# Performance work log

Measured on AMD Instinct MI355X. Metric: run time of the kernel, lower is better.

## Reference

```python
import jax, jax.numpy as jnp
import numpy as np
import math

IN_FEATURES = 1024
OUT_FEATURES = 1024
RANK = 16
ALPHA = 16.0
SCALING = ALPHA / RANK


def setup_inputs() -> dict:
    key = jax.random.key(0)
    k_x, k_w, k_b, k_a, k_bb = jax.random.split(key, 5)
    x = jax.random.normal(k_x, (8, 4096, IN_FEATURES), dtype=jnp.float32)
    # frozen linear params (W: [out, in], b: [out])
    W = jax.random.normal(k_w, (OUT_FEATURES, IN_FEATURES), dtype=jnp.float32) / math.sqrt(IN_FEATURES)
    b = jax.random.normal(k_b, (OUT_FEATURES,), dtype=jnp.float32) * 0.01
    # kaiming-uniform-like init for A; B nonzero here so the LoRA path is exercised
    bound = 1.0 / math.sqrt(IN_FEATURES)
    lora_A = jax.random.uniform(k_a, (RANK, IN_FEATURES), minval=-bound, maxval=bound, dtype=jnp.float32)
    lora_B = jax.random.normal(k_bb, (OUT_FEATURES, RANK), dtype=jnp.float32) * 0.02
    return {"x": x, "W": W, "b": b, "lora_A": lora_A, "lora_B": lora_B}


def reference(x, W, b, lora_A, lora_B):
    # y = x @ W^T + b + scaling * ((x @ A^T) @ B^T)
    # (mathematically identical to F.linear(x, B @ A); chained form avoids the
    #  full-rank [out, in] materialization)
    base = jnp.einsum("bsi,oi->bso", x, W) + b
    xa = jnp.einsum("bsi,ri->bsr", x, lora_A)      # [B, S, rank]
    lora_out = jnp.einsum("bsr,or->bso", xa, lora_B) * SCALING
    return base + lora_out
```

## Files before the change

kernel.cpp:

```cpp
#include <hip/hip_runtime.h>
#include <hip/hip_bf16.h>


typedef __bf16 bf16;
typedef bf16 bf16x8 __attribute__((ext_vector_type(8)));
typedef float f32x4 __attribute__((ext_vector_type(4)));

constexpr int K_DIM = 1024;
constexpr int N_DIM = 1024;
constexpr int M_DIM = 8 * 4096;
constexpr int NT = K_DIM / 64;
constexpr float SCALING = 16.0f / 16.0f;

__global__ __launch_bounds__(256) void weff_kernel(
    const float* __restrict__ W, const float* __restrict__ A,
    const float* __restrict__ B, bf16* __restrict__ weff) {
  const int o = blockIdx.x;
  const int tid = threadIdx.x;
  float br[16];
#pragma unroll
  for (int r = 0; r < 16; ++r) br[r] = B[o * 16 + r];
#pragma unroll
  for (int j = 0; j < 4; ++j) {
    const int k = tid + j * 256;
    float s = W[o * K_DIM + k];
#pragma unroll
    for (int r = 0; r < 16; ++r) s += SCALING * br[r] * A[r * K_DIM + k];
    weff[o * K_DIM + k] = (bf16)s;
  }
}

__device__ __forceinline__ void async16(const void* g, void* l) {
  __builtin_amdgcn_global_load_lds(
      (const __attribute__((address_space(1))) void*)g,
      (__attribute__((address_space(3))) void*)l, 16, 0, 0);
}
#define BAR() __builtin_amdgcn_s_barrier()
#define LGKM(n) asm volatile("s_waitcnt lgkmcnt(" #n ")" ::: "memory")
#define VMW(n) asm volatile("s_waitcnt vmcnt(" #n ")" ::: "memory")
#define MFMA(d, a, b) d = __builtin_amdgcn_mfma_f32_16x16x32_bf16(a, b, d, 0, 0, 0)


__global__ __launch_bounds__(512, 2) void gemm2b(
    const float* __restrict__ Xf, const bf16* __restrict__ Wf,
    const float* __restrict__ bias, float* __restrict__ Y) {
  __shared__ __align__(16) bf16 smem[65536];

  const int tid = threadIdx.x;
  const int lane = tid & 63;
  const int wid = tid >> 6;
  const int wm = wid >> 2;
  const int wn = wid & 3;
  const int l15 = lane & 15;
  const int lq = lane >> 4;

  const int bid = blockIdx.x;
  const int wgid = (bid & 7) * 64 + (bid >> 3);
  const int bm = wgid >> 2;
  const int bn = wgid & 3;
  const long m0 = (long)bm * 256;
  const int n0 = bn * 256;

  const int srow = tid >> 3;
  const int gch = (tid & 7) ^ (srow & 7);
  const bf16* wsrc = Wf + (long)(n0 + srow) * K_DIM + gch * 8;
  auto stageB = [&](int tt, int h) {
    bf16* dst = smem + (tt & 1) * 32768 + 16384 + h * 8192 + tid * 8;
    const bf16* s = wsrc + (long)h * 128 * K_DIM + tt * 64;
    async16(s, dst);
    async16(s + 64 * K_DIM, dst + 4096);
  };

  const int arow = tid >> 2;
  const int acp = tid & 3;
  const int ar7 = arow & 7;
  const int aslot0 = (2 * acp) ^ ar7;
  const int aslot1 = (2 * acp + 1) ^ ar7;
  const float* asrc = Xf + (m0 + arow) * K_DIM + acp * 16;

  f32x4 rA0[4], rA1[4];
  auto loadA0 = [&](int tt) {
    const float* s = asrc + tt * 64;
#pragma unroll
    for (int i = 0; i < 4; ++i) rA0[i] = *(const f32x4*)(s + i * 4);
  };
  auto loadA1 = [&](int tt) {
    const float* s = asrc + (long)128 * K_DIM + tt * 64;
#pragma unroll
    for (int i = 0; i < 4; ++i) rA1[i] = *(const f32x4*)(s + i * 4);
  };
  auto writeA0 = [&](int tt) {
    bf16* dst = smem + (tt & 1) * 32768 + arow * 64;
    bf16x8 c0, c1;
#pragma unroll
    for (int j = 0; j < 4; ++j) {
      c0[j] = (bf16)rA0[0][j];
      c0[4 + j] = (bf16)rA0[1][j];
      c1[j] = (bf16)rA0[2][j];
      c1[4 + j] = (bf16)rA0[3][j];
    }
    *(bf16x8*)(dst + aslot0 * 8) = c0;
    *(bf16x8*)(dst + aslot1 * 8) = c1;
  };
  auto writeA1 = [&](int tt) {
    bf16* dst = smem + (tt & 1) * 32768 + 8192 + arow * 64;
    bf16x8 c0, c1;
#pragma unroll
    for (int j = 0; j < 4; ++j) {
      c0[j] = (bf16)rA1[0][j];
      c0[4 + j] = (bf16)rA1[1][j];
      c1[j] = (bf16)rA1[2][j];
      c1[4 + j] = (bf16)rA1[3][j];
    }
    *(bf16x8*)(dst + aslot0 * 8) = c0;
    *(bf16x8*)(dst + aslot1 * 8) = c1;
  };

  const int key = l15 & 7;
  const int ck0 = lq ^ key;
  const int eA = (wm * 128 + l15) * 64 + ck0 * 8;
  const int eB = (wn * 64 + l15) * 64 + ck0 * 8;

  f32x4 acc[8][4] = {};

  loadA0(0); loadA1(0);
  stageB(0, 0); stageB(0, 1); stageB(1, 0); stageB(1, 1);
  writeA0(0); writeA1(0);
  loadA0(1); loadA1(1);
  VMW(12);
  LGKM(0);
  BAR();

  for (int t = 0; t < NT; ++t) {
    const bf16* Ab = smem + (t & 1) * 32768;
    const bf16* Bb = Ab + 16384;
    {
      bf16x8 B0[4], B1[4], A0[4], A1[4];
#pragma unroll
      for (int i = 0; i < 4; ++i) {
        B0[i] = *(const bf16x8*)(Bb + eB + i * 1024);
        B1[i] = *(const bf16x8*)(Bb + (eB ^ 32) + i * 1024);
        A0[i] = *(const bf16x8*)(Ab + eA + i * 1024);
        A1[i] = *(const bf16x8*)(Ab + (eA ^ 32) + i * 1024);
      }
      __builtin_amdgcn_s_setprio(1);
#pragma unroll
      for (int m = 0; m < 4; ++m)
#pragma unroll
        for (int n = 0; n < 4; ++n) MFMA(acc[m][n], A0[m], B0[n]);
#pragma unroll
      for (int m = 0; m < 4; ++m)
#pragma unroll
        for (int n = 0; n < 4; ++n) MFMA(acc[m][n], A1[m], B1[n]);
      __builtin_amdgcn_s_setprio(0);
      LGKM(0);
      BAR();
      bf16x8 C0[4], C1[4];
#pragma unroll
      for (int i = 0; i < 4; ++i) {
        C0[i] = *(const bf16x8*)(Ab + eA + 4096 + i * 1024);
        C1[i] = *(const bf16x8*)(Ab + (eA ^ 32) + 4096 + i * 1024);
      }
      if (t < NT - 2) { stageB(t + 2, 0); stageB(t + 2, 1); }
      if (t < NT - 1) { writeA0(t + 1); writeA1(t + 1); }
      if (t < NT - 2) { loadA0(t + 2); loadA1(t + 2); }
      __builtin_amdgcn_s_setprio(1);
#pragma unroll
      for (int m = 0; m < 4; ++m)
#pragma unroll
        for (int n = 0; n < 4; ++n) MFMA(acc[4 + m][n], C0[m], B0[n]);
#pragma unroll
      for (int m = 0; m < 4; ++m)
#pragma unroll
        for (int n = 0; n < 4; ++n) MFMA(acc[4 + m][n], C1[m], B1[n]);
      __builtin_amdgcn_s_setprio(0);
      LGKM(0);
      if (t < NT - 2) {
        VMW(12);
      } else if (t == NT - 2) {
        VMW(0);
      }
      BAR();
    }
  }

  const long crow0 = m0 + wm * 128 + lq * 4;
  const int ccol0 = n0 + wn * 64 + l15;
  float bn4[4];
#pragma unroll
  for (int n = 0; n < 4; ++n) bn4[n] = bias[ccol0 + n * 16];
#pragma unroll
  for (int m = 0; m < 8; ++m)
#pragma unroll
    for (int n = 0; n < 4; ++n) {
      const int col = ccol0 + n * 16;
#pragma unroll
      for (int i = 0; i < 4; ++i)
        Y[(crow0 + m * 16 + i) * N_DIM + col] = acc[m][n][i] + bn4[n];
    }
}

extern "C" void kernel_launch(void* const* d_in, const int* in_sizes, int n_in,
                              void* d_out, int out_size, void* d_ws, size_t ws_size,
                              hipStream_t stream) {
  const float* x = (const float*)d_in[0];
  const float* W = (const float*)d_in[1];
  const float* b = (const float*)d_in[2];
  const float* lA = (const float*)d_in[3];
  const float* lB = (const float*)d_in[4];
  float* y = (float*)d_out;

  bf16* weff = (bf16*)d_ws;

  weff_kernel<<<dim3(1024), dim3(256), 0, stream>>>(W, lA, lB, weff);

  const int grid = (M_DIM / 256) * (N_DIM / 256);
  gemm2b<<<dim3(grid), dim3(512), 0, stream>>>(x, weff, b, y);
}
```

Baseline: 100.5 us.

## Triple-buffer B tiles in LDS and use one barrier per K-step

Moves B-operand staging to a three-slot LDS ring, while A stays double-buffered. The prefetch of tile t+2 can now be issued at the top of each iteration into the slot freed by the previous step. All A and B fragments are read from LDS up front and all 64 MFMAs run back to back, so the mid-iteration barrier and LDS wait are gone. This targets synchronisation stalls between the two halves of the M tile, at the cost of 160KB of LDS per block and higher register pressure from holding every fragment at once.

```diff
diff --git a/kernel.cpp b/kernel.cpp
--- a/kernel.cpp
+++ b/kernel.cpp
@@ -41,10 +41,10 @@
 #define MFMA(d, a, b) d = __builtin_amdgcn_mfma_f32_16x16x32_bf16(a, b, d, 0, 0, 0)
 
 
-__global__ __launch_bounds__(512, 2) void gemm2b(
+__global__ __launch_bounds__(512, 2) void gemm1b(
     const float* __restrict__ Xf, const bf16* __restrict__ Wf,
     const float* __restrict__ bias, float* __restrict__ Y) {
-  __shared__ __align__(16) bf16 smem[65536];
+  __shared__ __align__(16) bf16 smem[81920];
 
   const int tid = threadIdx.x;
   const int lane = tid & 63;
@@ -64,8 +64,8 @@
   const int srow = tid >> 3;
   const int gch = (tid & 7) ^ (srow & 7);
   const bf16* wsrc = Wf + (long)(n0 + srow) * K_DIM + gch * 8;
-  auto stageB = [&](int tt, int h) {
-    bf16* dst = smem + (tt & 1) * 32768 + 16384 + h * 8192 + tid * 8;
+  auto stageB = [&](int tt, int h, int buf) {
+    bf16* dst = smem + 32768 + buf * 16384 + h * 8192 + tid * 8;
     const bf16* s = wsrc + (long)h * 128 * K_DIM + tt * 64;
     async16(s, dst);
     async16(s + 64 * K_DIM, dst + 4096);
@@ -90,7 +90,7 @@
     for (int i = 0; i < 4; ++i) rA1[i] = *(const f32x4*)(s + i * 4);
   };
   auto writeA0 = [&](int tt) {
-    bf16* dst = smem + (tt & 1) * 32768 + arow * 64;
+    bf16* dst = smem + (tt & 1) * 16384 + arow * 64;
     bf16x8 c0, c1;
 #pragma unroll
     for (int j = 0; j < 4; ++j) {
@@ -103,7 +103,7 @@
     *(bf16x8*)(dst + aslot1 * 8) = c1;
   };
   auto writeA1 = [&](int tt) {
-    bf16* dst = smem + (tt & 1) * 32768 + 8192 + arow * 64;
+    bf16* dst = smem + (tt & 1) * 16384 + 8192 + arow * 64;
     bf16x8 c0, c1;
 #pragma unroll
     for (int j = 0; j < 4; ++j) {
@@ -124,64 +124,64 @@
   f32x4 acc[8][4] = {};
 
   loadA0(0); loadA1(0);
-  stageB(0, 0); stageB(0, 1); stageB(1, 0); stageB(1, 1);
+  stageB(0, 0, 0); stageB(0, 1, 0);
+  stageB(1, 0, 1); stageB(1, 1, 1);
   writeA0(0); writeA1(0);
   loadA0(1); loadA1(1);
   VMW(12);
   LGKM(0);
   BAR();
 
+  int bR = 0;
   for (int t = 0; t < NT; ++t) {
-    const bf16* Ab = smem + (t & 1) * 32768;
-    const bf16* Bb = Ab + 16384;
-    {
-      bf16x8 B0[4], B1[4], A0[4], A1[4];
-#pragma unroll
-      for (int i = 0; i < 4; ++i) {
-        B0[i] = *(const bf16x8*)(Bb + eB + i * 1024);
-        B1[i] = *(const bf16x8*)(Bb + (eB ^ 32) + i * 1024);
-        A0[i] = *(const bf16x8*)(Ab + eA + i * 1024);
-        A1[i] = *(const bf16x8*)(Ab + (eA ^ 32) + i * 1024);
-      }
-      __builtin_amdgcn_s_setprio(1);
-#pragma unroll
-      for (int m = 0; m < 4; ++m)
-#pragma unroll
-        for (int n = 0; n < 4; ++n) MFMA(acc[m][n], A0[m], B0[n]);
-#pragma unroll
-      for (int m = 0; m < 4; ++m)
-#pragma unroll
-        for (int n = 0; n < 4; ++n) MFMA(acc[m][n], A1[m], B1[n]);
-      __builtin_amdgcn_s_setprio(0);
-      LGKM(0);
-      BAR();
-      bf16x8 C0[4], C1[4];
-#pragma unroll
-      for (int i = 0; i < 4; ++i) {
-        C0[i] = *(const bf16x8*)(Ab + eA + 4096 + i * 1024);
-        C1[i] = *(const bf16x8*)(Ab + (eA ^ 32) + 4096 + i * 1024);
-      }
-      if (t < NT - 2) { stageB(t + 2, 0); stageB(t + 2, 1); }
-      if (t < NT - 1) { writeA0(t + 1); writeA1(t + 1); }
-      if (t < NT - 2) { loadA0(t + 2); loadA1(t + 2); }
-      __builtin_amdgcn_s_setprio(1);
-#pragma unroll
-      for (int m = 0; m < 4; ++m)
-#pragma unroll
-        for (int n = 0; n < 4; ++n) MFMA(acc[4 + m][n], C0[m], B0[n]);
-#pragma unroll
-      for (int m = 0; m < 4; ++m)
-#pragma unroll
-        for (int n = 0; n < 4; ++n) MFMA(acc[4 + m][n], C1[m], B1[n]);
-      __builtin_amdgcn_s_setprio(0);
-      LGKM(0);
-      if (t < NT - 2) {
-        VMW(12);
-      } else if (t == NT - 2) {
-        VMW(0);
-      }
-      BAR();
-    }
+    const bf16* Ab = smem + (t & 1) * 16384;
+    const bf16* Bb = smem + 32768 + bR * 16384;
+    const int bW = (bR >= 1) ? bR - 1 : 2;
+
+    if (t < NT - 2) { stageB(t + 2, 0, bW); stageB(t + 2, 1, bW); }
+
+    bf16x8 A0[4], A1[4], C0[4], C1[4], B0[4], B1[4];
+#pragma unroll
+    for (int i = 0; i < 4; ++i) {
+      B0[i] = *(const bf16x8*)(Bb + eB + i * 1024);
+      B1[i] = *(const bf16x8*)(Bb + (eB ^ 32) + i * 1024);
+      A0[i] = *(const bf16x8*)(Ab + eA + i * 1024);
+      A1[i] = *(const bf16x8*)(Ab + (eA ^ 32) + i * 1024);
+      C0[i] = *(const bf16x8*)(Ab + eA + 4096 + i * 1024);
+      C1[i] = *(const bf16x8*)(Ab + (eA ^ 32) + 4096 + i * 1024);
+    }
+
+    if (t < NT - 1) { writeA0(t + 1); writeA1(t + 1); }
+    if (t < NT - 2) { loadA0(t + 2); loadA1(t + 2); }
+
+    __builtin_amdgcn_s_setprio(1);
+#pragma unroll
+    for (int m = 0; m < 4; ++m)
+#pragma unroll
+      for (int n = 0; n < 4; ++n) MFMA(acc[m][n], A0[m], B0[n]);
+#pragma unroll
+    for (int m = 0; m < 4; ++m)
+#pragma unroll
+      for (int n = 0; n < 4; ++n) MFMA(acc[m][n], A1[m], B1[n]);
+#pragma unroll
+    for (int m = 0; m < 4; ++m)
+#pragma unroll
+      for (int n = 0; n < 4; ++n) MFMA(acc[4 + m][n], C0[m], B0[n]);
+#pragma unroll
+    for (int m = 0; m < 4; ++m)
+#pragma unroll
+      for (int n = 0; n < 4; ++n) MFMA(acc[4 + m][n], C1[m], B1[n]);
+    __builtin_amdgcn_s_setprio(0);
+
+    LGKM(0);
+    if (t < NT - 2) {
+      VMW(12);
+    } else if (t == NT - 2) {
+      VMW(0);
+    }
+    BAR();
+
+    bR = (bR == 2) ? 0 : bR + 1;
   }
 
   const long crow0 = m0 + wm * 128 + lq * 4;
@@ -215,5 +215,5 @@
   weff_kernel<<<dim3(1024), dim3(256), 0, stream>>>(W, lA, lB, weff);
 
   const int grid = (M_DIM / 256) * (N_DIM / 256);
-  gemm2b<<<dim3(grid), dim3(512), 0, stream>>>(x, weff, b, y);
-}
+  gemm1b<<<dim3(grid), dim3(512), 0, stream>>>(x, weff, b, y);
+}
```

Measured after the change: 142.5 us. 1.42x slower.
